# Optimization experiments

Measured on AMD Instinct MI355X. Metric: run time of the kernel, lower is better.

## Reference

```python
import jax, jax.numpy as jnp
import numpy as np

B, T, D = 32, 1024, 1024
H = 512        # LSTM units per direction
L = 3          # num_layers


def _run_lstm(x, mask, W, U, b):
    """Masked unidirectional LSTM, Keras gate order (i, f, c, o).
    x: [B,T,D], mask: [B,T] bool (True = valid). Masked steps carry state
    and repeat the previous output, matching Keras masking semantics."""
    z_all = jnp.einsum('btd,dk->tbk', x, W) + b          # [T,B,4H]
    m_all = jnp.transpose(mask, (1, 0))                   # [T,B]

    def step(carry, inp):
        h, c = carry
        z_t, m_t = inp
        z = z_t + h @ U                                   # [B,4H]
        i, f, g, o = jnp.split(z, 4, axis=-1)
        i = jax.nn.sigmoid(i)
        f = jax.nn.sigmoid(f)
        g = jnp.tanh(g)
        o = jax.nn.sigmoid(o)
        c_new = f * c + i * g
        h_new = o * jnp.tanh(c_new)
        m = m_t[:, None]
        h = jnp.where(m, h_new, h)
        c = jnp.where(m, c_new, c)
        return (h, c), h

    h0 = jnp.zeros((x.shape[0], U.shape[0]), x.dtype)
    (_, _), hs = jax.lax.scan(step, (h0, h0), (z_all, m_all))
    return jnp.transpose(hs, (1, 0, 2))                   # [B,T,H]


def _bilstm(x, mask, Wf, Uf, bf, Wb, Ub, bb):
    fwd = _run_lstm(x, mask, Wf, Uf, bf)
    bwd = _run_lstm(x[:, ::-1], mask[:, ::-1], Wb, Ub, bb)[:, ::-1]
    return jnp.concatenate([fwd, bwd], axis=-1)           # [B,T,2H]


def setup_inputs() -> dict:
    key = jax.random.key(0)
    ks = jax.random.split(key, 16)
    s = 0.05
    inp = {
        'x': jax.random.normal(ks[0], (B, T, D), jnp.float32),
        'x_mask': jax.random.randint(ks[1], (B, T), 0, 2, jnp.int32),
        # stacked BiLSTM params (all layers share shapes since 2H == D)
        'Wf': jax.random.normal(ks[2], (L, D, 4 * H), jnp.float32) * s,
        'Uf': jax.random.normal(ks[3], (L, H, 4 * H), jnp.float32) * s,
        'bf': jax.random.normal(ks[4], (L, 4 * H), jnp.float32) * s,
        'Wb': jax.random.normal(ks[5], (L, D, 4 * H), jnp.float32) * s,
        'Ub': jax.random.normal(ks[6], (L, H, 4 * H), jnp.float32) * s,
        'bb': jax.random.normal(ks[7], (L, 4 * H), jnp.float32) * s,
        # task heads
        'Wp': jax.random.normal(ks[8], (2 * H, 2), jnp.float32) * s,
        'bp': jnp.zeros((2,), jnp.float32),
        'Wbu': jax.random.normal(ks[9], (2 * H, 2), jnp.float32) * s,
        'bbu': jnp.zeros((2,), jnp.float32),
        'Wss3': jax.random.normal(ks[10], (2 * H, 3), jnp.float32) * s,
        'bss3': jnp.zeros((3,), jnp.float32),
        'Wss8': jax.random.normal(ks[11], (2 * H, 8), jnp.float32) * s,
        'bss8': jnp.zeros((8,), jnp.float32),
        'training': 0,
    }
    return inp


def reference(x, x_mask, Wf, Uf, bf, Wb, Ub, bb, Wp, bp, Wbu, bbu,
              Wss3, bss3, Wss8, bss8, training):
    # mask = not(x_mask == 1): True = valid position
    mask = x_mask != 1
    for l in range(L):
        x = _bilstm(x, mask, Wf[l], Uf[l], bf[l], Wb[l], Ub[l], bb[l])
    x = jax.nn.relu(x)
    # dropout is identity at inference (training == 0)
    ppi = jax.nn.softmax(x @ Wp + bp, axis=-1)
    buried = x @ Wbu + bbu
    ss3 = x @ Wss3 + bss3
    ss8 = x @ Wss8 + bss8
    return (ppi, buried, ss3, ss8)
```

## Files before the change

kernel.cpp:

```cpp
#include <hip/hip_runtime.h>
#include <hip/hip_bf16.h>
#include <math.h>


#define B_ 32
#define T_ 1024
#define H_ 512
#define NG 2048

typedef __attribute__((ext_vector_type(8))) short bf16x8;
typedef __attribute__((ext_vector_type(4))) float f32x4;
typedef unsigned int u32;
typedef unsigned short u16;

__device__ inline u16 f2bf(float f) {
    u32 u = __float_as_uint(f);
    return (u16)((u + 0x7fffu + ((u >> 16) & 1u)) >> 16);
}
__device__ inline float bf2f(u16 v) { return __uint_as_float(((u32)v) << 16); }
__device__ inline void gload16(const void* g, void* l) {
    __builtin_amdgcn_global_load_lds(
        (const __attribute__((address_space(1))) u32*)g,
        (__attribute__((address_space(3))) u32*)l, 16, 0, 0);
}
__device__ inline float fsig(float x) { return 1.0f / (1.0f + __expf(-x)); }
__device__ inline float ftanh(float x) { return 1.0f - 2.0f / (__expf(2.0f * x) + 1.0f); }

__global__ void zero_mem(float* __restrict__ s, int n) {
    int i = blockIdx.x * 256 + threadIdx.x;
    if (i < n) s[i] = 0.0f;
}

__global__ __launch_bounds__(256) void conv_bf16(const float* __restrict__ src,
                                                 u16* __restrict__ dst) {
    int i = blockIdx.x * 256 + threadIdx.x;
    float4 v = *(const float4*)&src[(size_t)i * 4];
    ushort4 o = { f2bf(v.x), f2bf(v.y), f2bf(v.z), f2bf(v.w) };
    *(ushort4*)&dst[(size_t)i * 4] = o;
}

__global__ __launch_bounds__(256) void transpose_w(const float* __restrict__ Wf,
                                                   const float* __restrict__ Wb,
                                                   u16* __restrict__ wt) {
    int mat = blockIdx.z;
    const float* W = ((mat & 1) ? Wb : Wf) + (size_t)(mat >> 1) * 1024 * NG;
    u16* dst = wt + (size_t)mat * NG * 1024;
    __shared__ float tile[64][65];
    int n0 = blockIdx.x * 64, k0 = blockIdx.y * 64;
    int t = threadIdx.x;
#pragma unroll
    for (int i = 0; i < 16; ++i) {
        int idx = t + i * 256;
        int kk = idx >> 6, nn = idx & 63;
        tile[kk][nn] = W[(size_t)(k0 + kk) * NG + n0 + nn];
    }
    __syncthreads();
#pragma unroll
    for (int i = 0; i < 16; ++i) {
        int idx = t + i * 256;
        int nn = idx >> 6, kk = idx & 63;
        dst[(size_t)(n0 + nn) * 1024 + k0 + kk] = f2bf(tile[kk][nn]);
    }
}

__global__ __launch_bounds__(256) void pack_u(const float* __restrict__ Uf,
                                              const float* __restrict__ Ub,
                                              u16* __restrict__ upk) {
    int mat = blockIdx.y;
    const float* U = ((mat & 1) ? Ub : Uf) + (size_t)(mat >> 1) * H_ * NG;
    u16* dst = upk + (size_t)mat * 1048576;
    int f = blockIdx.x * 256 + threadIdx.x;
    int lane = f & 63, ks = (f >> 6) & 15, c2 = (f >> 10) & 1;
    int cp = (f >> 11) & 3, wg = f >> 13;
    int col = cp * H_ + wg * 32 + c2 * 16 + (lane & 15);
    int krow = ks * 32 + (lane >> 4) * 8;
    u16 o[8];
#pragma unroll
    for (int j = 0; j < 8; ++j) o[j] = f2bf(U[(size_t)(krow + j) * NG + col]);
    *(uint4*)(dst + (size_t)f * 8) = *(uint4*)o;
}

__global__ __launch_bounds__(256) void gemm_mfma(
    const u16* __restrict__ A, const u16* __restrict__ Bt,
    const float* __restrict__ bias, u16* __restrict__ Zb,
    int t0, int lgC) {
    __shared__ __align__(16) u16 sA[128 * 32];
    __shared__ __align__(16) u16 sB[128 * 32];
    const int tid = threadIdx.x;
    const int m0 = blockIdx.y * 128, n0 = blockIdx.x * 128;
    const int Cmask = (1 << lgC) - 1;

    const int chunk0 = tid, chunk1 = tid + 256;
    const int r0 = chunk0 >> 2, kp0 = (chunk0 & 3) * 8;
    const int r1 = chunk1 >> 2, kp1 = (chunk1 & 3) * 8;
    const int gm0 = m0 + r0, gm1 = m0 + r1;
    const size_t arow0 = ((size_t)(gm0 >> lgC) * T_ + t0 + (gm0 & Cmask)) * 1024;
    const size_t arow1 = ((size_t)(gm1 >> lgC) * T_ + t0 + (gm1 & Cmask)) * 1024;
    const size_t brow0 = (size_t)(n0 + r0) * 1024;
    const size_t brow1 = (size_t)(n0 + r1) * 1024;

    const int lane = tid & 63, wave = tid >> 6;
    const int wr = (wave >> 1) * 64, wc = (wave & 1) * 64;
    const int fr = lane & 15, fk = (lane >> 4) * 8;

    f32x4 acc[4][4] = {};
    for (int kc = 0; kc < 1024; kc += 32) {
        gload16(A + arow0 + kc + kp0, &sA[chunk0 * 8]);
        gload16(A + arow1 + kc + kp1, &sA[chunk1 * 8]);
        gload16(Bt + brow0 + kc + kp0, &sB[chunk0 * 8]);
        gload16(Bt + brow1 + kc + kp1, &sB[chunk1 * 8]);
        __syncthreads();
        bf16x8 af[4], bfr[4];
#pragma unroll
        for (int i = 0; i < 4; ++i)
            af[i] = *(const bf16x8*)&sA[(wr + i * 16 + fr) * 32 + fk];
#pragma unroll
        for (int j = 0; j < 4; ++j)
            bfr[j] = *(const bf16x8*)&sB[(wc + j * 16 + fr) * 32 + fk];
#pragma unroll
        for (int i = 0; i < 4; ++i)
#pragma unroll
            for (int j = 0; j < 4; ++j)
                acc[i][j] = __builtin_amdgcn_mfma_f32_16x16x32_bf16(
                    af[i], bfr[j], acc[i][j], 0, 0, 0);
        __syncthreads();
    }
    float bv[4];
    int un[4], gn[4];
#pragma unroll
    for (int j = 0; j < 4; ++j) {
        int n = n0 + wc + j * 16 + fr;
        bv[j] = bias[n];
        un[j] = n & 511; gn[j] = n >> 9;
    }
#pragma unroll
    for (int i = 0; i < 4; ++i) {
        int mb = m0 + wr + i * 16 + (lane >> 4) * 4;
#pragma unroll
        for (int j = 0; j < 4; ++j) {
#pragma unroll
            for (int r = 0; r < 4; ++r)
                Zb[(size_t)(mb + r) * 2048 + un[j] * 4 + gn[j]] =
                    f2bf(acc[i][j][r] + bv[j]);
        }
    }
}

__global__ __launch_bounds__(512, 1) void lstm_chunk(
    const u16* __restrict__ zf, const u16* __restrict__ zb,
    const u16* __restrict__ upk,
    const int* __restrict__ xmask,
    u32* __restrict__ hbuf32,
    float* __restrict__ cst, float* __restrict__ hst,
    u32* __restrict__ flags,
    u16* __restrict__ hseq,
    int t0f, int t0b, int C, int sbase) {
    const int bx = blockIdx.x, dir = bx >> 4, wgs = bx & 15, u0 = wgs * 32;
    const u16* z = dir ? zb : zf;
    const u16* up = upk + dir * 1048576;
    u32* hb32 = hbuf32 + dir * 16384;
    u32* myflag = flags + dir * 16 + wgs;
    const u32* fbase = flags + dir * 16;
    const int tid = threadIdx.x;
    const int wave = tid >> 6, lane = tid & 63;
    const int cp = wave & 3, bt = wave >> 2, fr = lane & 15, fq = lane >> 4;
    const int row = bt * 16 + fr;
    const int swz = (row & 7) << 4;

    __shared__ __align__(16) u16 sh[16384];
    __shared__ float sacc[32 * 132];

    bf16x8 uf0[16], uf1[16];
#pragma unroll
    for (int ks = 0; ks < 16; ++ks) {
        size_t base0 = (((size_t)(wgs * 4 + cp) * 2) * 16 + ks) * 512 + lane * 8;
        uf0[ks] = *(const bf16x8*)(up + base0);
        uf1[ks] = *(const bf16x8*)(up + base0 + 16 * 512);
    }

    const int b0p = tid >> 5, ul = tid & 31, b1p = b0p + 16, ug = u0 + ul;
    const int sidx = (dir * 16 + wgs) * 1024 + tid * 2;
    float c0r = cst[sidx], c1r = cst[sidx + 1];
    float h0r = hst[sidx], h1r = hst[sidx + 1];
    const size_t hs0 = (size_t)b0p * T_ * 1024 + dir * 512 + ug;
    const size_t hs1 = (size_t)b1p * T_ * 1024 + dir * 512 + ug;

    {
        u32 tmp[16];
#pragma unroll
        for (int k = 0; k < 16; ++k)
            tmp[k] = __hip_atomic_load(hb32 + k * 512 + tid, __ATOMIC_RELAXED,
                                       __HIP_MEMORY_SCOPE_AGENT);
#pragma unroll
        for (int k = 0; k < 16; ++k) {
            int idx = k * 512 + tid;
            int sb = (idx * 4) ^ (((idx >> 8) & 7) << 4);
            *(u32*)((char*)sh + sb) = tmp[k];
        }
    }
    ushort4 za0, za1; int mc0, mc1;
    {
        int tc = dir ? (C - 1) : 0;
        int t = dir ? (t0b + C - 1) : t0f;
        za0 = *(const ushort4*)(z + ((size_t)(b0p * C + tc)) * 2048 + ug * 4);
        za1 = *(const ushort4*)(z + ((size_t)(b1p * C + tc)) * 2048 + ug * 4);
        mc0 = xmask[b0p * T_ + t]; mc1 = xmask[b1p * T_ + t];
    }
    __syncthreads();

    u16 hb0s = 0, hb1s = 0;
    for (int st = 0; st < C; ++st) {
        const int t = dir ? (t0b + C - 1 - st) : (t0f + st);
        u32* nx32 = hb32 + (((st & 1) ^ 1) ? 8192 : 0);

        f32x4 acc0 = {0, 0, 0, 0}, acc1 = {0, 0, 0, 0};
#pragma unroll
        for (int ks = 0; ks < 16; ++ks) {
            int abyte = (row * 1024 + ks * 64 + fq * 16) ^ swz;
            bf16x8 a = *(const bf16x8*)((const char*)sh + abyte);
            acc0 = __builtin_amdgcn_mfma_f32_16x16x32_bf16(a, uf0[ks], acc0, 0, 0, 0);
            acc1 = __builtin_amdgcn_mfma_f32_16x16x32_bf16(a, uf1[ks], acc1, 0, 0, 0);
        }
#pragma unroll
        for (int j = 0; j < 4; ++j) {
            int b = bt * 16 + fq * 4 + j;
            sacc[b * 132 + cp * 32 + fr] = acc0[j];
            sacc[b * 132 + cp * 32 + 16 + fr] = acc1[j];
        }
        __syncthreads();
        {
            const float* s0 = sacc + b0p * 132;
            const float* s1 = sacc + b1p * 132;
            float i0 = fsig(bf2f(za0.x) + s0[ul]);
            float f0 = fsig(bf2f(za0.y) + s0[32 + ul]);
            float g0 = ftanh(bf2f(za0.z) + s0[64 + ul]);
            float o0 = fsig(bf2f(za0.w) + s0[96 + ul]);
            if (mc0 != 1) { c0r = f0 * c0r + i0 * g0; h0r = o0 * ftanh(c0r); }
            float i1 = fsig(bf2f(za1.x) + s1[ul]);
            float f1 = fsig(bf2f(za1.y) + s1[32 + ul]);
            float g1 = ftanh(bf2f(za1.z) + s1[64 + ul]);
            float o1 = fsig(bf2f(za1.w) + s1[96 + ul]);
            if (mc1 != 1) { c1r = f1 * c1r + i1 * g1; h1r = o1 * ftanh(c1r); }
            hb0s = f2bf(h0r); hb1s = f2bf(h1r);
            u32 nb0 = __shfl_xor((u32)hb0s, 1, 64);
            u32 nb1 = __shfl_xor((u32)hb1s, 1, 64);
            if ((ul & 1) == 0) {
                u32 pk0 = (u32)hb0s | (nb0 << 16);
                u32 pk1 = (u32)hb1s | (nb1 << 16);
                __hip_atomic_store(nx32 + b0p * 256 + (ug >> 1), pk0,
                                   __ATOMIC_RELAXED, __HIP_MEMORY_SCOPE_AGENT);
                __hip_atomic_store(nx32 + b1p * 256 + (ug >> 1), pk1,
                                   __ATOMIC_RELAXED, __HIP_MEMORY_SCOPE_AGENT);
            }
        }
        __syncthreads();
        const u32 tgt = (u32)(sbase + st + 1);
        if (tid == 0)
            __hip_atomic_store(myflag, tgt, __ATOMIC_RELAXED,
                               __HIP_MEMORY_SCOPE_AGENT);
        hseq[hs0 + (size_t)t * 1024] = hb0s;
        hseq[hs1 + (size_t)t * 1024] = hb1s;
        ushort4 zn0, zn1; int mn0, mn1;
        {
            int stn = (st + 1 < C) ? st + 1 : st;
            int tcn = dir ? (C - 1 - stn) : stn;
            int tn = dir ? (t0b + tcn) : (t0f + tcn);
            zn0 = *(const ushort4*)(z + ((size_t)(b0p * C + tcn)) * 2048 + ug * 4);
            zn1 = *(const ushort4*)(z + ((size_t)(b1p * C + tcn)) * 2048 + ug * 4);
            mn0 = xmask[b0p * T_ + tn]; mn1 = xmask[b1p * T_ + tn];
        }
        {
            u32 v = 0xffffffffu;
            if (lane < 16)
                v = __hip_atomic_load(fbase + lane, __ATOMIC_RELAXED,
                                      __HIP_MEMORY_SCOPE_AGENT);
            while (!__all(v >= tgt)) {
                if (lane < 16)
                    v = __hip_atomic_load(fbase + lane, __ATOMIC_RELAXED,
                                          __HIP_MEMORY_SCOPE_AGENT);
            }
        }
        if (st + 1 < C) {
            const u32* src = hb32 + (((st + 1) & 1) ? 8192 : 0);
            u32 tmp[16];
#pragma unroll
            for (int k = 0; k < 16; ++k)
                tmp[k] = __hip_atomic_load(src + k * 512 + tid, __ATOMIC_RELAXED,
                                           __HIP_MEMORY_SCOPE_AGENT);
#pragma unroll
            for (int k = 0; k < 16; ++k) {
                int idx = k * 512 + tid;
                int sb = (idx * 4) ^ (((idx >> 8) & 7) << 4);
                *(u32*)((char*)sh + sb) = tmp[k];
            }
        }
        za0 = zn0; za1 = zn1; mc0 = mn0; mc1 = mn1;
        __syncthreads();
    }
    cst[sidx] = c0r; cst[sidx + 1] = c1r;
    hst[sidx] = h0r; hst[sidx + 1] = h1r;
}

__global__ __launch_bounds__(256) void heads_kernel(
    const u16* __restrict__ xin,
    const float* __restrict__ Wp, const float* __restrict__ bp,
    const float* __restrict__ Wbu, const float* __restrict__ bbu,
    const float* __restrict__ Wss3, const float* __restrict__ bss3,
    const float* __restrict__ Wss8, const float* __restrict__ bss8,
    float* __restrict__ out) {
    const int r = blockIdx.x * 4 + (threadIdx.x >> 6);
    const int lane = threadIdx.x & 63;
    const u16* xr = xin + (size_t)r * 1024 + lane * 16;
    uint4 q0 = *(const uint4*)xr;
    uint4 q1 = *(const uint4*)(xr + 8);
    float xv[16];
    u32 qs[8] = { q0.x, q0.y, q0.z, q0.w, q1.x, q1.y, q1.z, q1.w };
#pragma unroll
    for (int i = 0; i < 8; ++i) {
        xv[i * 2]     = fmaxf(__uint_as_float((qs[i] & 0xffffu) << 16), 0.0f);
        xv[i * 2 + 1] = fmaxf(__uint_as_float(qs[i] & 0xffff0000u), 0.0f);
    }
    float acc[15] = {};
    const int k0 = lane * 16;
#pragma unroll
    for (int kk = 0; kk < 16; kk++) {
        float xk = xv[kk];
        int k = k0 + kk;
        acc[0] += xk * Wp[k * 2];      acc[1] += xk * Wp[k * 2 + 1];
        acc[2] += xk * Wbu[k * 2];     acc[3] += xk * Wbu[k * 2 + 1];
        acc[4] += xk * Wss3[k * 3];    acc[5] += xk * Wss3[k * 3 + 1];
        acc[6] += xk * Wss3[k * 3 + 2];
#pragma unroll
        for (int o = 0; o < 8; o++) acc[7 + o] += xk * Wss8[k * 8 + o];
    }
#pragma unroll
    for (int o = 0; o < 15; o++) {
#pragma unroll
        for (int off = 32; off; off >>= 1) acc[o] += __shfl_xor(acc[o], off, 64);
    }
    if (lane == 0) {
        float a0 = acc[0] + bp[0], a1 = acc[1] + bp[1];
        float mx = fmaxf(a0, a1);
        float e0 = expf(a0 - mx), e1 = expf(a1 - mx);
        float ssum = e0 + e1;
        out[(size_t)r * 2] = e0 / ssum;
        out[(size_t)r * 2 + 1] = e1 / ssum;
        float* ob = out + 65536;
        ob[r * 2] = acc[2] + bbu[0]; ob[r * 2 + 1] = acc[3] + bbu[1];
        float* o3 = out + 131072;
        o3[r * 3 + 0] = acc[4] + bss3[0];
        o3[r * 3 + 1] = acc[5] + bss3[1];
        o3[r * 3 + 2] = acc[6] + bss3[2];
        float* o8 = out + 229376;
#pragma unroll
        for (int o = 0; o < 8; o++) o8[r * 8 + o] = acc[7 + o] + bss8[o];
    }
}

extern "C" void kernel_launch(void* const* d_in, const int* in_sizes, int n_in,
                              void* d_out, int out_size, void* d_ws, size_t ws_size,
                              hipStream_t stream) {
    const float* x = (const float*)d_in[0];
    const int* xmask = (const int*)d_in[1];
    const float* Wf = (const float*)d_in[2];
    const float* Uf = (const float*)d_in[3];
    const float* bfp = (const float*)d_in[4];
    const float* Wb = (const float*)d_in[5];
    const float* Ub = (const float*)d_in[6];
    const float* bbp = (const float*)d_in[7];
    const float* Wp = (const float*)d_in[8];
    const float* bp = (const float*)d_in[9];
    const float* Wbu = (const float*)d_in[10];
    const float* bbu = (const float*)d_in[11];
    const float* Wss3 = (const float*)d_in[12];
    const float* bss3 = (const float*)d_in[13];
    const float* Wss8 = (const float*)d_in[14];
    const float* bss8 = (const float*)d_in[15];

    char* wsb = (char*)d_ws;
    u16* actA = (u16*)wsb;
    u16* actB = (u16*)(wsb + (64ull << 20));
    u16* wt   = (u16*)(wsb + (128ull << 20));
    u16* upk  = (u16*)(wsb + (152ull << 20));
    char* stb = wsb + (164ull << 20);
    u32* hbuf32 = (u32*)stb;
    float* cst = (float*)(stb + 131072);
    float* hst = (float*)(stb + 262144);
    u32* flags = (u32*)(stb + 393216);
    const int stateFloats = (393216 + 128) / 4;

    size_t fixedB = 165ull << 20;
    int C = 1024;
    while (C > 128 && fixedB + 262144ull * C > ws_size) C >>= 1;
    int lgC = 31 - __builtin_clz((unsigned)C);
    u16* zf = (u16*)(wsb + fixedB);
    u16* zb = zf + (size_t)B_ * C * 2048;

    conv_bf16<<<dim3(8388608 / 256), 256, 0, stream>>>(x, actA);
    transpose_w<<<dim3(32, 16, 6), 256, 0, stream>>>(Wf, Wb, wt);
    pack_u<<<dim3(512, 6), 256, 0, stream>>>(Uf, Ub, upk);

    const u16* cur = actA;
    for (int l = 0; l < 3; l++) {
        u16* dst = (l & 1) ? actA : actB;
        zero_mem<<<dim3((stateFloats + 255) / 256), 256, 0, stream>>>(
            (float*)stb, stateFloats);
        u16* wtf = wt + (size_t)(l * 2 + 0) * NG * 1024;
        u16* wtb = wt + (size_t)(l * 2 + 1) * NG * 1024;
        const u16* upkl = upk + (size_t)l * 2 * 1048576;
        const float* bfl = bfp + l * NG;
        const float* bbl = bbp + l * NG;
        for (int c0 = 0; c0 < T_; c0 += C) {
            int t0f = c0;
            int t0b = T_ - c0 - C;
            dim3 ggrid(NG / 128, (B_ * C) / 128);
            gemm_mfma<<<ggrid, 256, 0, stream>>>(cur, wtf, bfl, zf, t0f, lgC);
            gemm_mfma<<<ggrid, 256, 0, stream>>>(cur, wtb, bbl, zb, t0b, lgC);

            const u16* a_zf = zf; const u16* a_zb = zb;
            const u16* a_up = upkl; const int* a_xm = xmask;
            u32* a_hb = hbuf32; float* a_cs = cst; float* a_hs = hst;
            u32* a_fl = flags; u16* a_hseq = dst;
            int a_t0f = t0f, a_t0b = t0b, a_C = C, a_sb = c0;
            void* kargs[] = { &a_zf, &a_zb, &a_up, &a_xm, &a_hb, &a_cs, &a_hs,
                              &a_fl, &a_hseq, &a_t0f, &a_t0b, &a_C, &a_sb };
            hipLaunchCooperativeKernel((void*)lstm_chunk, dim3(32), dim3(512),
                                       kargs, 0, stream);
        }
        cur = dst;
    }
    heads_kernel<<<dim3(B_ * T_ / 4), 256, 0, stream>>>(
        cur, Wp, bp, Wbu, bbu, Wss3, bss3, Wss8, bss8, (float*)d_out);
}
```

Before: 11.79 ms.

## Permute recurrent weight packing so gate outputs land in registers, dropping LDS staging

Repacks the recurrent weight matrix so each MFMA output lane holds all four gates (i,f,g,o) of one unit for one batch row, swapping the MFMA operand order. This lets the LSTM cell update consume the accumulators directly, removing the shared-memory scratch buffer, its stores and loads, and one block-wide barrier per timestep on the serial critical path. The z-gate loads and hidden-state stores are remapped to match, with each thread writing one packed word instead of needing a cross-lane shuffle. The per-thread state mapping changes, so the carried c/h state layout in global memory must stay consistent across chunk launches.

```diff
diff --git a/kernel.cpp b/kernel.cpp
--- a/kernel.cpp
+++ b/kernel.cpp
@@ -72,11 +72,15 @@
     int f = blockIdx.x * 256 + threadIdx.x;
     int lane = f & 63, ks = (f >> 6) & 15, c2 = (f >> 10) & 1;
     int cp = (f >> 11) & 3, wg = f >> 13;
-    int col = cp * H_ + wg * 32 + c2 * 16 + (lane & 15);
-    int krow = ks * 32 + (lane >> 4) * 8;
+    int r = lane & 15, kb = lane >> 4;
+    int col = (r & 3) * H_ + wg * 32 + cp * 8 + c2 * 4 + (r >> 2);
+    int kbase = ks * 32 + kb * 8;
     u16 o[8];
 #pragma unroll
-    for (int j = 0; j < 8; ++j) o[j] = f2bf(U[(size_t)(krow + j) * NG + col]);
+    for (int j = 0; j < 8; ++j) {
+        int k = kbase + (j & 1) * 4 + (j >> 1);
+        o[j] = f2bf(U[(size_t)k * NG + col]);
+    }
     *(uint4*)(dst + (size_t)f * 8) = *(uint4*)o;
 }
 
@@ -168,7 +172,6 @@
     const int swz = (row & 7) << 4;
 
     __shared__ __align__(16) u16 sh[16384];
-    __shared__ float sacc[32 * 132];
 
     bf16x8 uf0[16], uf1[16];
 #pragma unroll
@@ -178,12 +181,13 @@
         uf1[ks] = *(const bf16x8*)(up + base0 + 16 * 512);
     }
 
-    const int b0p = tid >> 5, ul = tid & 31, b1p = b0p + 16, ug = u0 + ul;
+    const int ua = u0 + cp * 8 + fq;
+    const int ub2 = ua + 4;
     const int sidx = (dir * 16 + wgs) * 1024 + tid * 2;
-    float c0r = cst[sidx], c1r = cst[sidx + 1];
-    float h0r = hst[sidx], h1r = hst[sidx + 1];
-    const size_t hs0 = (size_t)b0p * T_ * 1024 + dir * 512 + ug;
-    const size_t hs1 = (size_t)b1p * T_ * 1024 + dir * 512 + ug;
+    float ca = cst[sidx], cb = cst[sidx + 1];
+    float ha = hst[sidx], hb2 = hst[sidx + 1];
+    const size_t hsA = (size_t)row * T_ * 1024 + dir * 512 + ua;
+    const int hword = row * 256 + wgs * 16 + cp * 4 + fq;
 
     {
         u32 tmp[16];
@@ -198,17 +202,18 @@
             *(u32*)((char*)sh + sb) = tmp[k];
         }
     }
-    ushort4 za0, za1; int mc0, mc1;
+    ushort4 zA, zB; int mc;
     {
         int tc = dir ? (C - 1) : 0;
         int t = dir ? (t0b + C - 1) : t0f;
-        za0 = *(const ushort4*)(z + ((size_t)(b0p * C + tc)) * 2048 + ug * 4);
-        za1 = *(const ushort4*)(z + ((size_t)(b1p * C + tc)) * 2048 + ug * 4);
-        mc0 = xmask[b0p * T_ + t]; mc1 = xmask[b1p * T_ + t];
+        const u16* zr = z + ((size_t)(row * C + tc)) * 2048;
+        zA = *(const ushort4*)(zr + ua * 4);
+        zB = *(const ushort4*)(zr + ub2 * 4);
+        mc = xmask[row * T_ + t];
     }
     __syncthreads();
 
-    u16 hb0s = 0, hb1s = 0;
+    u16 h16a = 0, h16b = 0;
     for (int st = 0; st < C; ++st) {
         const int t = dir ? (t0b + C - 1 - st) : (t0f + st);
         u32* nx32 = hb32 + (((st & 1) ^ 1) ? 8192 : 0);
@@ -217,57 +222,42 @@
 #pragma unroll
         for (int ks = 0; ks < 16; ++ks) {
             int abyte = (row * 1024 + ks * 64 + fq * 16) ^ swz;
-            bf16x8 a = *(const bf16x8*)((const char*)sh + abyte);
-            acc0 = __builtin_amdgcn_mfma_f32_16x16x32_bf16(a, uf0[ks], acc0, 0, 0, 0);
-            acc1 = __builtin_amdgcn_mfma_f32_16x16x32_bf16(a, uf1[ks], acc1, 0, 0, 0);
-        }
-#pragma unroll
-        for (int j = 0; j < 4; ++j) {
-            int b = bt * 16 + fq * 4 + j;
-            sacc[b * 132 + cp * 32 + fr] = acc0[j];
-            sacc[b * 132 + cp * 32 + 16 + fr] = acc1[j];
-        }
-        __syncthreads();
+            bf16x8 b = *(const bf16x8*)((const char*)sh + abyte);
+            acc0 = __builtin_amdgcn_mfma_f32_16x16x32_bf16(uf0[ks], b, acc0, 0, 0, 0);
+            acc1 = __builtin_amdgcn_mfma_f32_16x16x32_bf16(uf1[ks], b, acc1, 0, 0, 0);
+        }
         {
-            const float* s0 = sacc + b0p * 132;
-            const float* s1 = sacc + b1p * 132;
-            float i0 = fsig(bf2f(za0.x) + s0[ul]);
-            float f0 = fsig(bf2f(za0.y) + s0[32 + ul]);
-            float g0 = ftanh(bf2f(za0.z) + s0[64 + ul]);
-            float o0 = fsig(bf2f(za0.w) + s0[96 + ul]);
-            if (mc0 != 1) { c0r = f0 * c0r + i0 * g0; h0r = o0 * ftanh(c0r); }
-            float i1 = fsig(bf2f(za1.x) + s1[ul]);
-            float f1 = fsig(bf2f(za1.y) + s1[32 + ul]);
-            float g1 = ftanh(bf2f(za1.z) + s1[64 + ul]);
-            float o1 = fsig(bf2f(za1.w) + s1[96 + ul]);
-            if (mc1 != 1) { c1r = f1 * c1r + i1 * g1; h1r = o1 * ftanh(c1r); }
-            hb0s = f2bf(h0r); hb1s = f2bf(h1r);
-            u32 nb0 = __shfl_xor((u32)hb0s, 1, 64);
-            u32 nb1 = __shfl_xor((u32)hb1s, 1, 64);
-            if ((ul & 1) == 0) {
-                u32 pk0 = (u32)hb0s | (nb0 << 16);
-                u32 pk1 = (u32)hb1s | (nb1 << 16);
-                __hip_atomic_store(nx32 + b0p * 256 + (ug >> 1), pk0,
-                                   __ATOMIC_RELAXED, __HIP_MEMORY_SCOPE_AGENT);
-                __hip_atomic_store(nx32 + b1p * 256 + (ug >> 1), pk1,
-                                   __ATOMIC_RELAXED, __HIP_MEMORY_SCOPE_AGENT);
-            }
+            float i0 = fsig(bf2f(zA.x) + acc0[0]);
+            float f0 = fsig(bf2f(zA.y) + acc0[1]);
+            float g0 = ftanh(bf2f(zA.z) + acc0[2]);
+            float o0 = fsig(bf2f(zA.w) + acc0[3]);
+            if (mc != 1) { ca = f0 * ca + i0 * g0; ha = o0 * ftanh(ca); }
+            float i1 = fsig(bf2f(zB.x) + acc1[0]);
+            float f1 = fsig(bf2f(zB.y) + acc1[1]);
+            float g1 = ftanh(bf2f(zB.z) + acc1[2]);
+            float o1 = fsig(bf2f(zB.w) + acc1[3]);
+            if (mc != 1) { cb = f1 * cb + i1 * g1; hb2 = o1 * ftanh(cb); }
+            h16a = f2bf(ha); h16b = f2bf(hb2);
+            u32 pk = (u32)h16a | ((u32)h16b << 16);
+            __hip_atomic_store(nx32 + hword, pk,
+                               __ATOMIC_RELAXED, __HIP_MEMORY_SCOPE_AGENT);
         }
         __syncthreads();
         const u32 tgt = (u32)(sbase + st + 1);
         if (tid == 0)
             __hip_atomic_store(myflag, tgt, __ATOMIC_RELAXED,
                                __HIP_MEMORY_SCOPE_AGENT);
-        hseq[hs0 + (size_t)t * 1024] = hb0s;
-        hseq[hs1 + (size_t)t * 1024] = hb1s;
-        ushort4 zn0, zn1; int mn0, mn1;
+        hseq[hsA + (size_t)t * 1024] = h16a;
+        hseq[hsA + 4 + (size_t)t * 1024] = h16b;
+        ushort4 znA, znB; int mn;
         {
             int stn = (st + 1 < C) ? st + 1 : st;
             int tcn = dir ? (C - 1 - stn) : stn;
             int tn = dir ? (t0b + tcn) : (t0f + tcn);
-            zn0 = *(const ushort4*)(z + ((size_t)(b0p * C + tcn)) * 2048 + ug * 4);
-            zn1 = *(const ushort4*)(z + ((size_t)(b1p * C + tcn)) * 2048 + ug * 4);
-            mn0 = xmask[b0p * T_ + tn]; mn1 = xmask[b1p * T_ + tn];
+            const u16* zr = z + ((size_t)(row * C + tcn)) * 2048;
+            znA = *(const ushort4*)(zr + ua * 4);
+            znB = *(const ushort4*)(zr + ub2 * 4);
+            mn = xmask[row * T_ + tn];
         }
         {
             u32 v = 0xffffffffu;
@@ -294,11 +284,11 @@
                 *(u32*)((char*)sh + sb) = tmp[k];
             }
         }
-        za0 = zn0; za1 = zn1; mc0 = mn0; mc1 = mn1;
+        zA = znA; zB = znB; mc = mn;
         __syncthreads();
     }
-    cst[sidx] = c0r; cst[sidx + 1] = c1r;
-    hst[sidx] = h0r; hst[sidx + 1] = h1r;
+    cst[sidx] = ca; cst[sidx + 1] = cb;
+    hst[sidx] = ha; hst[sidx + 1] = hb2;
 }
 
 __global__ __launch_bounds__(256) void heads_kernel(
```

After: 13.57 ms. +15.2%, slower.

## Fuse input-projection GEMM with recurrent LSTM in one cooperative kernel

Applied to the files above, without the earlier changes.

Replaces the per-chunk GEMM launches plus the cooperative recurrent kernel with a single cooperative kernel per layer. 224 producer workgroups compute the input projections in time-block order, forward blocks ascending and backward blocks descending, and bump per-block counters. The 32 recurrent workgroups spin on those counters before reading each time block's gate inputs. The aim is to overlap the large input GEMM with the latency-bound recurrence and to drop launch and serialization costs. The risks are reduced GEMM throughput from fewer, smaller-tile workgroups, extra spin-wait overhead, and a requirement that all 256 workgroups be co-resident.

```diff
diff --git a/kernel.cpp b/kernel.cpp
--- a/kernel.cpp
+++ b/kernel.cpp
@@ -11,6 +11,7 @@
 typedef __attribute__((ext_vector_type(8))) short bf16x8;
 typedef __attribute__((ext_vector_type(4))) float f32x4;
 typedef unsigned int u32;
+typedef unsigned long long u64;
 typedef unsigned short u16;
 
 __device__ inline u16 f2bf(float f) {
@@ -80,95 +81,104 @@
     *(uint4*)(dst + (size_t)f * 8) = *(uint4*)o;
 }
 
-__global__ __launch_bounds__(256) void gemm_mfma(
-    const u16* __restrict__ A, const u16* __restrict__ Bt,
-    const float* __restrict__ bias, u16* __restrict__ Zb,
-    int t0, int lgC) {
-    __shared__ __align__(16) u16 sA[128 * 32];
-    __shared__ __align__(16) u16 sB[128 * 32];
-    const int tid = threadIdx.x;
-    const int m0 = blockIdx.y * 128, n0 = blockIdx.x * 128;
-    const int Cmask = (1 << lgC) - 1;
-
-    const int chunk0 = tid, chunk1 = tid + 256;
-    const int r0 = chunk0 >> 2, kp0 = (chunk0 & 3) * 8;
-    const int r1 = chunk1 >> 2, kp1 = (chunk1 & 3) * 8;
-    const int gm0 = m0 + r0, gm1 = m0 + r1;
-    const size_t arow0 = ((size_t)(gm0 >> lgC) * T_ + t0 + (gm0 & Cmask)) * 1024;
-    const size_t arow1 = ((size_t)(gm1 >> lgC) * T_ + t0 + (gm1 & Cmask)) * 1024;
-    const size_t brow0 = (size_t)(n0 + r0) * 1024;
-    const size_t brow1 = (size_t)(n0 + r1) * 1024;
-
-    const int lane = tid & 63, wave = tid >> 6;
-    const int wr = (wave >> 1) * 64, wc = (wave & 1) * 64;
-    const int fr = lane & 15, fk = (lane >> 4) * 8;
-
-    f32x4 acc[4][4] = {};
-    for (int kc = 0; kc < 1024; kc += 32) {
-        gload16(A + arow0 + kc + kp0, &sA[chunk0 * 8]);
-        gload16(A + arow1 + kc + kp1, &sA[chunk1 * 8]);
-        gload16(Bt + brow0 + kc + kp0, &sB[chunk0 * 8]);
-        gload16(Bt + brow1 + kc + kp1, &sB[chunk1 * 8]);
-        __syncthreads();
-        bf16x8 af[4], bfr[4];
-#pragma unroll
-        for (int i = 0; i < 4; ++i)
-            af[i] = *(const bf16x8*)&sA[(wr + i * 16 + fr) * 32 + fk];
-#pragma unroll
-        for (int j = 0; j < 4; ++j)
-            bfr[j] = *(const bf16x8*)&sB[(wc + j * 16 + fr) * 32 + fk];
-#pragma unroll
-        for (int i = 0; i < 4; ++i)
-#pragma unroll
-            for (int j = 0; j < 4; ++j)
-                acc[i][j] = __builtin_amdgcn_mfma_f32_16x16x32_bf16(
-                    af[i], bfr[j], acc[i][j], 0, 0, 0);
-        __syncthreads();
-    }
-    float bv[4];
-    int un[4], gn[4];
-#pragma unroll
-    for (int j = 0; j < 4; ++j) {
-        int n = n0 + wc + j * 16 + fr;
-        bv[j] = bias[n];
-        un[j] = n & 511; gn[j] = n >> 9;
-    }
-#pragma unroll
-    for (int i = 0; i < 4; ++i) {
-        int mb = m0 + wr + i * 16 + (lane >> 4) * 4;
-#pragma unroll
-        for (int j = 0; j < 4; ++j) {
-#pragma unroll
-            for (int r = 0; r < 4; ++r)
-                Zb[(size_t)(mb + r) * 2048 + un[j] * 4 + gn[j]] =
-                    f2bf(acc[i][j][r] + bv[j]);
-        }
-    }
-}
-
-__global__ __launch_bounds__(512, 1) void lstm_chunk(
-    const u16* __restrict__ zf, const u16* __restrict__ zb,
+__global__ __launch_bounds__(512, 1) void fused_layer(
+    const u16* __restrict__ act,
+    const u16* __restrict__ wtf, const u16* __restrict__ wtb,
+    const float* __restrict__ bfl, const float* __restrict__ bbl,
+    u16* __restrict__ zf, u16* __restrict__ zb,
     const u16* __restrict__ upk,
     const int* __restrict__ xmask,
     u32* __restrict__ hbuf32,
     float* __restrict__ cst, float* __restrict__ hst,
     u32* __restrict__ flags,
-    u16* __restrict__ hseq,
-    int t0f, int t0b, int C, int sbase) {
-    const int bx = blockIdx.x, dir = bx >> 4, wgs = bx & 15, u0 = wgs * 32;
-    const u16* z = dir ? zb : zf;
+    u32* __restrict__ cnt,
+    u16* __restrict__ hseq) {
+    const int bx = blockIdx.x;
+    const int tid = threadIdx.x;
+    const int wave = tid >> 6, lane = tid & 63;
+    const int fr = lane & 15, fq = lane >> 4;
+
+    __shared__ __align__(16) u16 sh[16384];
+    __shared__ float sacc[32 * 132];
+
+    if (bx >= 32) {
+        const int g = bx - 32;
+        const int dir = (g >= 112) ? 1 : 0;
+        const int local = dir ? g - 112 : g;
+        const u16* Bt = dir ? wtb : wtf;
+        const float* bias = dir ? bbl : bfl;
+        u16* Zb = dir ? zb : zf;
+        u32* mycnt = cnt + dir * 8;
+        u16* sA = sh;
+        u16* sB = sh + 4096;
+        const int r = tid >> 2, kp = (tid & 3) * 8;
+        const int wr = (wave & 1) * 64, wc = (wave >> 1) * 32;
+        for (int i = local; i < 4096; i += 112) {
+            int tb_ord = i >> 9, within = i & 511;
+            int b = within >> 4, nt = within & 15;
+            int tb = dir ? 7 - tb_ord : tb_ord;
+            int m0 = b * 1024 + tb * 128;
+            int n0 = nt * 128;
+            const size_t arow = (size_t)(m0 + r) * 1024;
+            const size_t brow = (size_t)(n0 + r) * 1024;
+            f32x4 acc[4][2] = {};
+            for (int kc = 0; kc < 1024; kc += 32) {
+                gload16(act + arow + kc + kp, sA + tid * 8);
+                gload16(Bt + brow + kc + kp, sB + tid * 8);
+                __syncthreads();
+                bf16x8 af[4], bfr[2];
+                const int fk = fq * 8;
+#pragma unroll
+                for (int ii = 0; ii < 4; ++ii)
+                    af[ii] = *(const bf16x8*)&sA[(wr + ii * 16 + fr) * 32 + fk];
+#pragma unroll
+                for (int j = 0; j < 2; ++j)
+                    bfr[j] = *(const bf16x8*)&sB[(wc + j * 16 + fr) * 32 + fk];
+#pragma unroll
+                for (int ii = 0; ii < 4; ++ii)
+#pragma unroll
+                    for (int j = 0; j < 2; ++j)
+                        acc[ii][j] = __builtin_amdgcn_mfma_f32_16x16x32_bf16(
+                            af[ii], bfr[j], acc[ii][j], 0, 0, 0);
+                __syncthreads();
+            }
+            float bv[2]; int un[2], gn[2];
+#pragma unroll
+            for (int j = 0; j < 2; ++j) {
+                int n = n0 + wc + j * 16 + fr;
+                bv[j] = bias[n];
+                un[j] = n & 511; gn[j] = n >> 9;
+            }
+#pragma unroll
+            for (int ii = 0; ii < 4; ++ii) {
+                int mb = m0 + wr + ii * 16 + fq * 4;
+#pragma unroll
+                for (int j = 0; j < 2; ++j)
+#pragma unroll
+                    for (int rr = 0; rr < 4; ++rr)
+                        Zb[(size_t)(mb + rr) * 2048 + un[j] * 4 + gn[j]] =
+                            f2bf(acc[ii][j][rr] + bv[j]);
+            }
+            __syncthreads();
+            if (tid == 0) {
+                __threadfence();
+                __hip_atomic_fetch_add(mycnt + tb, 1u, __ATOMIC_RELAXED,
+                                       __HIP_MEMORY_SCOPE_AGENT);
+            }
+        }
+        return;
+    }
+
+    const int dir = bx >> 4, wgs = bx & 15, u0 = wgs * 32;
+    const u64* z64 = (const u64*)(dir ? zb : zf);
     const u16* up = upk + dir * 1048576;
     u32* hb32 = hbuf32 + dir * 16384;
     u32* myflag = flags + dir * 16 + wgs;
     const u32* fbase = flags + dir * 16;
-    const int tid = threadIdx.x;
-    const int wave = tid >> 6, lane = tid & 63;
-    const int cp = wave & 3, bt = wave >> 2, fr = lane & 15, fq = lane >> 4;
+    const u32* ctb = cnt + dir * 8;
+    const int cp = wave & 3, bt = wave >> 2;
     const int row = bt * 16 + fr;
     const int swz = (row & 7) << 4;
-
-    __shared__ __align__(16) u16 sh[16384];
-    __shared__ float sacc[32 * 132];
 
     bf16x8 uf0[16], uf1[16];
 #pragma unroll
@@ -185,6 +195,20 @@
     const size_t hs0 = (size_t)b0p * T_ * 1024 + dir * 512 + ug;
     const size_t hs1 = (size_t)b1p * T_ * 1024 + dir * 512 + ug;
 
+    int haveb = -1;
+    auto wait_tb = [&](int tb) {
+        if (tb == haveb) return;
+        const u32* cpp = ctb + tb;
+        u32 v = 512;
+        if (lane == 0) v = __hip_atomic_load(cpp, __ATOMIC_RELAXED,
+                                             __HIP_MEMORY_SCOPE_AGENT);
+        while (!__all(v >= 512)) {
+            if (lane == 0) v = __hip_atomic_load(cpp, __ATOMIC_RELAXED,
+                                                 __HIP_MEMORY_SCOPE_AGENT);
+        }
+        haveb = tb;
+    };
+
     {
         u32 tmp[16];
 #pragma unroll
@@ -198,19 +222,21 @@
             *(u32*)((char*)sh + sb) = tmp[k];
         }
     }
-    ushort4 za0, za1; int mc0, mc1;
+    u64 za0, za1; int mc0, mc1;
     {
-        int tc = dir ? (C - 1) : 0;
-        int t = dir ? (t0b + C - 1) : t0f;
-        za0 = *(const ushort4*)(z + ((size_t)(b0p * C + tc)) * 2048 + ug * 4);
-        za1 = *(const ushort4*)(z + ((size_t)(b1p * C + tc)) * 2048 + ug * 4);
-        mc0 = xmask[b0p * T_ + t]; mc1 = xmask[b1p * T_ + t];
+        int tc = dir ? (T_ - 1) : 0;
+        wait_tb(tc >> 7);
+        za0 = __hip_atomic_load(z64 + (size_t)(b0p * T_ + tc) * 512 + ug,
+                                __ATOMIC_RELAXED, __HIP_MEMORY_SCOPE_AGENT);
+        za1 = __hip_atomic_load(z64 + (size_t)(b1p * T_ + tc) * 512 + ug,
+                                __ATOMIC_RELAXED, __HIP_MEMORY_SCOPE_AGENT);
+        mc0 = xmask[b0p * T_ + tc]; mc1 = xmask[b1p * T_ + tc];
     }
     __syncthreads();
 
     u16 hb0s = 0, hb1s = 0;
-    for (int st = 0; st < C; ++st) {
-        const int t = dir ? (t0b + C - 1 - st) : (t0f + st);
+    for (int st = 0; st < T_; ++st) {
+        const int t = dir ? (T_ - 1 - st) : st;
         u32* nx32 = hb32 + (((st & 1) ^ 1) ? 8192 : 0);
 
         f32x4 acc0 = {0, 0, 0, 0}, acc1 = {0, 0, 0, 0};
@@ -231,15 +257,15 @@
         {
             const float* s0 = sacc + b0p * 132;
             const float* s1 = sacc + b1p * 132;
-            float i0 = fsig(bf2f(za0.x) + s0[ul]);
-            float f0 = fsig(bf2f(za0.y) + s0[32 + ul]);
-            float g0 = ftanh(bf2f(za0.z) + s0[64 + ul]);
-            float o0 = fsig(bf2f(za0.w) + s0[96 + ul]);
+            float i0 = fsig(bf2f((u16)za0) + s0[ul]);
+            float f0 = fsig(bf2f((u16)(za0 >> 16)) + s0[32 + ul]);
+            float g0 = ftanh(bf2f((u16)(za0 >> 32)) + s0[64 + ul]);
+            float o0 = fsig(bf2f((u16)(za0 >> 48)) + s0[96 + ul]);
             if (mc0 != 1) { c0r = f0 * c0r + i0 * g0; h0r = o0 * ftanh(c0r); }
-            float i1 = fsig(bf2f(za1.x) + s1[ul]);
-            float f1 = fsig(bf2f(za1.y) + s1[32 + ul]);
-            float g1 = ftanh(bf2f(za1.z) + s1[64 + ul]);
-            float o1 = fsig(bf2f(za1.w) + s1[96 + ul]);
+            float i1 = fsig(bf2f((u16)za1) + s1[ul]);
+            float f1 = fsig(bf2f((u16)(za1 >> 16)) + s1[32 + ul]);
+            float g1 = ftanh(bf2f((u16)(za1 >> 32)) + s1[64 + ul]);
+            float o1 = fsig(bf2f((u16)(za1 >> 48)) + s1[96 + ul]);
             if (mc1 != 1) { c1r = f1 * c1r + i1 * g1; h1r = o1 * ftanh(c1r); }
             hb0s = f2bf(h0r); hb1s = f2bf(h1r);
             u32 nb0 = __shfl_xor((u32)hb0s, 1, 64);
@@ -254,20 +280,22 @@
             }
         }
         __syncthreads();
-        const u32 tgt = (u32)(sbase + st + 1);
+        const u32 tgt = (u32)(st + 1);
         if (tid == 0)
             __hip_atomic_store(myflag, tgt, __ATOMIC_RELAXED,
                                __HIP_MEMORY_SCOPE_AGENT);
         hseq[hs0 + (size_t)t * 1024] = hb0s;
         hseq[hs1 + (size_t)t * 1024] = hb1s;
-        ushort4 zn0, zn1; int mn0, mn1;
+        u64 zn0 = 0, zn1 = 0; int mn0 = 0, mn1 = 0;
         {
-            int stn = (st + 1 < C) ? st + 1 : st;
-            int tcn = dir ? (C - 1 - stn) : stn;
-            int tn = dir ? (t0b + tcn) : (t0f + tcn);
-            zn0 = *(const ushort4*)(z + ((size_t)(b0p * C + tcn)) * 2048 + ug * 4);
-            zn1 = *(const ushort4*)(z + ((size_t)(b1p * C + tcn)) * 2048 + ug * 4);
-            mn0 = xmask[b0p * T_ + tn]; mn1 = xmask[b1p * T_ + tn];
+            int stn = (st + 1 < T_) ? st + 1 : st;
+            int tcn = dir ? (T_ - 1 - stn) : stn;
+            wait_tb(tcn >> 7);
+            zn0 = __hip_atomic_load(z64 + (size_t)(b0p * T_ + tcn) * 512 + ug,
+                                    __ATOMIC_RELAXED, __HIP_MEMORY_SCOPE_AGENT);
+            zn1 = __hip_atomic_load(z64 + (size_t)(b1p * T_ + tcn) * 512 + ug,
+                                    __ATOMIC_RELAXED, __HIP_MEMORY_SCOPE_AGENT);
+            mn0 = xmask[b0p * T_ + tcn]; mn1 = xmask[b1p * T_ + tcn];
         }
         {
             u32 v = 0xffffffffu;
@@ -280,7 +308,7 @@
                                           __HIP_MEMORY_SCOPE_AGENT);
             }
         }
-        if (st + 1 < C) {
+        if (st + 1 < T_) {
             const u32* src = hb32 + (((st + 1) & 1) ? 8192 : 0);
             u32 tmp[16];
 #pragma unroll
@@ -387,14 +415,12 @@
     float* cst = (float*)(stb + 131072);
     float* hst = (float*)(stb + 262144);
     u32* flags = (u32*)(stb + 393216);
-    const int stateFloats = (393216 + 128) / 4;
+    u32* cnt   = (u32*)(stb + 393344);
+    const int stateFloats = (393344 + 64) / 4;
 
     size_t fixedB = 165ull << 20;
-    int C = 1024;
-    while (C > 128 && fixedB + 262144ull * C > ws_size) C >>= 1;
-    int lgC = 31 - __builtin_clz((unsigned)C);
     u16* zf = (u16*)(wsb + fixedB);
-    u16* zb = zf + (size_t)B_ * C * 2048;
+    u16* zb = zf + (size_t)B_ * T_ * 2048;
 
     conv_bf16<<<dim3(8388608 / 256), 256, 0, stream>>>(x, actA);
     transpose_w<<<dim3(32, 16, 6), 256, 0, stream>>>(Wf, Wb, wt);
@@ -410,23 +436,19 @@
         const u16* upkl = upk + (size_t)l * 2 * 1048576;
         const float* bfl = bfp + l * NG;
         const float* bbl = bbp + l * NG;
-        for (int c0 = 0; c0 < T_; c0 += C) {
-            int t0f = c0;
-            int t0b = T_ - c0 - C;
-            dim3 ggrid(NG / 128, (B_ * C) / 128);
-            gemm_mfma<<<ggrid, 256, 0, stream>>>(cur, wtf, bfl, zf, t0f, lgC);
-            gemm_mfma<<<ggrid, 256, 0, stream>>>(cur, wtb, bbl, zb, t0b, lgC);
-
-            const u16* a_zf = zf; const u16* a_zb = zb;
-            const u16* a_up = upkl; const int* a_xm = xmask;
-            u32* a_hb = hbuf32; float* a_cs = cst; float* a_hs = hst;
-            u32* a_fl = flags; u16* a_hseq = dst;
-            int a_t0f = t0f, a_t0b = t0b, a_C = C, a_sb = c0;
-            void* kargs[] = { &a_zf, &a_zb, &a_up, &a_xm, &a_hb, &a_cs, &a_hs,
-                              &a_fl, &a_hseq, &a_t0f, &a_t0b, &a_C, &a_sb };
-            hipLaunchCooperativeKernel((void*)lstm_chunk, dim3(32), dim3(512),
-                                       kargs, 0, stream);
-        }
+
+        const u16* a_act = cur;
+        const u16* a_wtf = wtf; const u16* a_wtb = wtb;
+        const float* a_bf = bfl; const float* a_bb = bbl;
+        u16* a_zf = zf; u16* a_zb = zb;
+        const u16* a_up = upkl; const int* a_xm = xmask;
+        u32* a_hb = hbuf32; float* a_cs = cst; float* a_hs = hst;
+        u32* a_fl = flags; u32* a_cnt = cnt; u16* a_hseq = dst;
+        void* kargs[] = { &a_act, &a_wtf, &a_wtb, &a_bf, &a_bb, &a_zf, &a_zb,
+                          &a_up, &a_xm, &a_hb, &a_cs, &a_hs, &a_fl, &a_cnt,
+                          &a_hseq };
+        hipLaunchCooperativeKernel((void*)fused_layer, dim3(256), dim3(512),
+                                   kargs, 0, stream);
         cur = dst;
     }
     heads_kernel<<<dim3(B_ * T_ / 4), 256, 0, stream>>>(
```

New measurement: 12.20 ms. 3.5% more time.
